# Optimization experiments

Measured on AMD Instinct MI355X. Metric: run time of the kernel, lower is better.

## Reference

```python
import jax, jax.numpy as jnp
import numpy as np


def swiglu(g, u):
    return jax.nn.silu(g) * u


def setup_inputs() -> dict:
    key = jax.random.key(0)
    ks = jax.random.split(key, 10)
    D, H, E, HS = 2048, 512, 32, 1024
    B, S = 1, 2048
    s = 0.02
    return {
        "x": jax.random.normal(ks[0], (B, S, D), jnp.float32),
        "gate_w": jax.random.normal(ks[1], (E, D), jnp.float32) * s,
        "expert_bias": jnp.zeros((E,), jnp.float32),
        "wg": jax.random.normal(ks[2], (E, D, H), jnp.float32) * s,
        "wu": jax.random.normal(ks[3], (E, D, H), jnp.float32) * s,
        "wd": jax.random.normal(ks[4], (E, H, D), jnp.float32) * s,
        "sg": jax.random.normal(ks[5], (D, HS), jnp.float32) * s,
        "su": jax.random.normal(ks[6], (D, HS), jnp.float32) * s,
        "sd": jax.random.normal(ks[7], (HS, D), jnp.float32) * s,
        "coef_w": jax.random.normal(ks[8], (2, D), jnp.float32) * s,
        "coef_b": jnp.zeros((2,), jnp.float32),
        "top_k": 4,
    }


def reference(x, gate_w, expert_bias, wg, wu, wd, sg, su, sd, coef_w, coef_b, top_k):
    # --- sigmoid router with bias-adjusted top-k selection ---
    logits = jnp.einsum("bsd,ed->bse", x, gate_w)            # [B,S,E]
    routing = jax.nn.sigmoid(logits.astype(jnp.float32))
    biased = routing + expert_bias[None, None, :]
    _, inds = jax.lax.top_k(biased, top_k)                    # [B,S,k]
    scores = jnp.take_along_axis(routing, inds, axis=-1)      # gather UNbiased weights
    scores = scores / (jnp.sum(scores, axis=-1, keepdims=True) + 1e-20)  # norm_topk_prob
    scores = scores.astype(x.dtype)

    # --- SwitchGLU experts: dense per-expert SwiGLU, then gather top-k outputs ---
    h = jnp.einsum("bsd,edh->bseh", x, wg)                    # [B,S,E,H]
    u = jnp.einsum("bsd,edh->bseh", x, wu)
    y_all = jnp.einsum("bseh,ehd->bsed", swiglu(h, u), wd)    # [B,S,E,D]
    expert_out = jnp.take_along_axis(
        y_all, inds[..., None], axis=2)                        # [B,S,k,D]
    y_experts = jnp.sum(expert_out * scores[..., None], axis=-2)  # [B,S,D]

    # --- shared expert + learned 2-way mixing coefficient ---
    shared = swiglu(x @ sg, x @ su) @ sd                      # [B,S,D]
    coef = jax.nn.softmax(jnp.einsum("bsd,cd->bsc", x, coef_w) + coef_b, axis=-1)
    return y_experts * coef[..., :1] + shared * coef[..., 1:]
```

## Files before the change

### kernel.cpp

```cpp
#include <hip/hip_runtime.h>
#include <hip/hip_bf16.h>
#include <stdint.h>

#define S_TOK   2048
#define DMODEL  2048
#define HEXP    512
#define NEXP    32
#define HSH     1024
#define NPAIR   (S_TOK * 4)
#define MAXTILES 96

#define META_NT  0
#define META_TE  1
#define META_TP0 (1 + MAXTILES)
#define META_TM  (1 + 2 * MAXTILES)
#define META_SIZE (1 + 3 * MAXTILES)

typedef short  s16x8 __attribute__((ext_vector_type(8)));
typedef __bf16 b16x8 __attribute__((ext_vector_type(8)));
typedef float  f32x4 __attribute__((ext_vector_type(4)));

__device__ __forceinline__ f32x4 mfma16x16x32(s16x8 a, s16x8 b, f32x4 c) {
    return __builtin_amdgcn_mfma_f32_16x16x32_bf16(
        __builtin_bit_cast(b16x8, a), __builtin_bit_cast(b16x8, b), c, 0, 0, 0);
}

__device__ __forceinline__ unsigned short f2bf(float f) {
    union { float f; unsigned int u; } v; v.f = f;
    unsigned int u = v.u;
    return (unsigned short)((u + 0x7FFFu + ((u >> 16) & 1u)) >> 16);
}

__global__ __launch_bounds__(256)
void router_kernel(const float* __restrict__ x, const float* __restrict__ gate_w,
                   const float* __restrict__ expert_bias,
                   const float* __restrict__ coef_w, const float* __restrict__ coef_b,
                   int* __restrict__ inds, float* __restrict__ scores,
                   float* __restrict__ coefo)
{
    const int t = blockIdx.x;
    const int tid = threadIdx.x;
    const int lane = tid & 63;
    const int wave = tid >> 6;
    const float* xr = x + (size_t)t * DMODEL;

    float xv[32];
#pragma unroll
    for (int j = 0; j < 32; ++j) xv[j] = xr[lane + 64 * j];

    __shared__ float s_logits[NEXP];
    __shared__ float s_coef[2];

    for (int i = 0; i < 8; ++i) {
        const int e = wave * 8 + i;
        const float* wr = gate_w + (size_t)e * DMODEL;
        float p = 0.f;
#pragma unroll
        for (int j = 0; j < 32; ++j) p += xv[j] * wr[lane + 64 * j];
#pragma unroll
        for (int o = 32; o > 0; o >>= 1) p += __shfl_xor(p, o);
        if (lane == 0) s_logits[e] = p;
    }
    if (wave == 0) {
        for (int c = 0; c < 2; ++c) {
            const float* wr = coef_w + (size_t)c * DMODEL;
            float p = 0.f;
#pragma unroll
            for (int j = 0; j < 32; ++j) p += xv[j] * wr[lane + 64 * j];
#pragma unroll
            for (int o = 32; o > 0; o >>= 1) p += __shfl_xor(p, o);
            if (lane == 0) s_coef[c] = p;
        }
    }
    __syncthreads();
    if (tid == 0) {
        float routing[NEXP], biased[NEXP];
        for (int e = 0; e < NEXP; ++e) {
            const float r = 1.f / (1.f + expf(-s_logits[e]));
            routing[e] = r;
            biased[e] = r + expert_bias[e];
        }
        int sel[4]; float sc[4]; float ssum = 0.f;
        for (int k = 0; k < 4; ++k) {
            int best = 0; float bv = -1e30f;
            for (int e = 0; e < NEXP; ++e)
                if (biased[e] > bv) { bv = biased[e]; best = e; }
            sel[k] = best; sc[k] = routing[best]; ssum += sc[k];
            biased[best] = -1e30f;
        }
        const float inv = 1.f / (ssum + 1e-20f);
        for (int k = 0; k < 4; ++k) {
            inds[t * 4 + k] = sel[k];
            scores[t * 4 + k] = sc[k] * inv;
        }
        const float l0 = s_coef[0] + coef_b[0];
        const float l1 = s_coef[1] + coef_b[1];
        const float m = fmaxf(l0, l1);
        const float e0 = expf(l0 - m), e1 = expf(l1 - m);
        coefo[t * 2 + 0] = e0 / (e0 + e1);
        coefo[t * 2 + 1] = e1 / (e0 + e1);
    }
}

__global__ __launch_bounds__(256)
void xcast_kernel(const float* __restrict__ x, unsigned short* __restrict__ xb)
{
    const int i = (blockIdx.x * 256 + threadIdx.x) * 4;
    const float4 v = *reinterpret_cast<const float4*>(x + i);
    ushort4 o;
    o.x = f2bf(v.x); o.y = f2bf(v.y); o.z = f2bf(v.z); o.w = f2bf(v.w);
    *reinterpret_cast<ushort4*>(xb + i) = o;
}

__global__ __launch_bounds__(1024)
void group_kernel(const int* __restrict__ inds, const float* __restrict__ scores,
                  int* __restrict__ meta, int* __restrict__ pair_token,
                  float* __restrict__ pair_score)
{
    __shared__ int cnt[NEXP];
    __shared__ int off_s[NEXP];
    __shared__ int cur[NEXP];
    const int tid = threadIdx.x;
    if (tid < NEXP) cnt[tid] = 0;
    __syncthreads();
    for (int i = tid; i < NPAIR; i += 1024) atomicAdd(&cnt[inds[i]], 1);
    __syncthreads();
    if (tid == 0) {
        int run = 0, nt = 0;
        for (int e = 0; e < NEXP; ++e) {
            off_s[e] = run;
            const int c = cnt[e];
            for (int m0 = 0; m0 < c; m0 += 128) {
                meta[META_TE + nt] = e;
                meta[META_TP0 + nt] = run + m0;
                meta[META_TM + nt] = (c - m0 < 128) ? (c - m0) : 128;
                ++nt;
            }
            run += c;
        }
        meta[META_NT] = nt;
    }
    __syncthreads();
    if (tid < NEXP) cur[tid] = off_s[tid];
    __syncthreads();
    for (int i = tid; i < NPAIR; i += 1024) {
        const int e = inds[i];
        const int pos = atomicAdd(&cur[e], 1);
        pair_token[pos] = i >> 2;
        pair_score[pos] = scores[i];
    }
}

template <bool GATHER>
__global__ __launch_bounds__(256, 2)
void gateup_kernel(const unsigned short* __restrict__ xb,
                   const float* __restrict__ Bg_all, const float* __restrict__ Bu_all,
                   unsigned short* __restrict__ act,
                   const int* __restrict__ meta, const int* __restrict__ pair_token,
                   const int NB)
{
    __shared__ unsigned short Al[128][40];
    __shared__ unsigned short Bgl[64][40];
    __shared__ unsigned short Bul[64][40];

    const int tid = threadIdx.x;
    int p0, mval;
    const float *Bg, *Bu;
    if constexpr (GATHER) {
        const int tt = blockIdx.y;
        if (tt >= meta[META_NT]) return;
        const int e = meta[META_TE + tt];
        p0 = meta[META_TP0 + tt];
        mval = meta[META_TM + tt];
        const size_t eoff = (size_t)e * DMODEL * NB;
        Bg = Bg_all + eoff;
        Bu = Bu_all + eoff;
    } else {
        p0 = blockIdx.y * 128;
        mval = 128;
        Bg = Bg_all;
        Bu = Bu_all;
    }
    const int n0 = blockIdx.x * 64;

    const int am = tid >> 1;
    const int ah = (tid & 1) * 16;
    int tok;
    if constexpr (GATHER) {
        int p = p0 + am; if (p > NPAIR - 1) p = NPAIR - 1;
        tok = pair_token[p];
    } else {
        tok = p0 + am;
    }
    const unsigned short* asrc = xb + (size_t)tok * DMODEL + ah;

    const int bn = tid & 63;
    const int bk = (tid >> 6) * 8;
    const float* bgsrc = Bg + (size_t)bk * NB + (n0 + bn);
    const float* busrc = Bu + (size_t)bk * NB + (n0 + bn);

    uint4 av0 = *reinterpret_cast<const uint4*>(asrc);
    uint4 av1 = *reinterpret_cast<const uint4*>(asrc + 8);
    float pg[8], pu[8];
#pragma unroll
    for (int j = 0; j < 8; ++j) {
        pg[j] = bgsrc[(size_t)j * NB];
        pu[j] = busrc[(size_t)j * NB];
    }

    const f32x4 zero4 = {0.f, 0.f, 0.f, 0.f};
    f32x4 hacc[4][2], uacc[4][2];
#pragma unroll
    for (int m = 0; m < 4; ++m)
#pragma unroll
        for (int n = 0; n < 2; ++n) { hacc[m][n] = zero4; uacc[m][n] = zero4; }

    const int lane = tid & 63;
    const int wave = tid >> 6;
    const int wm = wave >> 1, wn = wave & 1;
    const int fr = lane & 15;
    const int fk = (lane >> 4) * 8;

    for (int k0 = 0; k0 < DMODEL; k0 += 32) {
        __syncthreads();
        *reinterpret_cast<uint4*>(&Al[am][ah])     = av0;
        *reinterpret_cast<uint4*>(&Al[am][ah + 8]) = av1;
        union { unsigned short us[8]; uint4 v; } wg_, wu_;
#pragma unroll
        for (int j = 0; j < 8; ++j) { wg_.us[j] = f2bf(pg[j]); wu_.us[j] = f2bf(pu[j]); }
        *reinterpret_cast<uint4*>(&Bgl[bn][bk]) = wg_.v;
        *reinterpret_cast<uint4*>(&Bul[bn][bk]) = wu_.v;
        if (k0 + 32 < DMODEL) {
            av0 = *reinterpret_cast<const uint4*>(asrc + k0 + 32);
            av1 = *reinterpret_cast<const uint4*>(asrc + k0 + 40);
            const float* g2 = bgsrc + (size_t)(k0 + 32) * NB;
            const float* u2 = busrc + (size_t)(k0 + 32) * NB;
#pragma unroll
            for (int j = 0; j < 8; ++j) { pg[j] = g2[(size_t)j * NB]; pu[j] = u2[(size_t)j * NB]; }
        }
        __syncthreads();

        s16x8 af[4], bgf[2], buf2[2];
#pragma unroll
        for (int m = 0; m < 4; ++m)
            af[m] = *reinterpret_cast<const s16x8*>(&Al[wm * 64 + m * 16 + fr][fk]);
#pragma unroll
        for (int n = 0; n < 2; ++n) {
            bgf[n]  = *reinterpret_cast<const s16x8*>(&Bgl[wn * 32 + n * 16 + fr][fk]);
            buf2[n] = *reinterpret_cast<const s16x8*>(&Bul[wn * 32 + n * 16 + fr][fk]);
        }
#pragma unroll
        for (int m = 0; m < 4; ++m)
#pragma unroll
            for (int n = 0; n < 2; ++n) {
                hacc[m][n] = mfma16x16x32(af[m], bgf[n], hacc[m][n]);
                uacc[m][n] = mfma16x16x32(af[m], buf2[n], uacc[m][n]);
            }
    }

#pragma unroll
    for (int m = 0; m < 4; ++m)
#pragma unroll
        for (int n = 0; n < 2; ++n) {
            const int col = n0 + wn * 32 + n * 16 + fr;
#pragma unroll
            for (int r = 0; r < 4; ++r) {
                const int rt = wm * 64 + m * 16 + (lane >> 4) * 4 + r;
                if (rt < mval) {
                    const float hv = hacc[m][n][r];
                    const float a = hv / (1.f + __expf(-hv)) * uacc[m][n][r];
                    act[(size_t)(p0 + rt) * NB + col] = f2bf(a);
                }
            }
        }
}

template <bool EXPERT>
__global__ __launch_bounds__(256, 2)
void down_kernel(const unsigned short* __restrict__ act,
                 const float* __restrict__ Bd_all,
                 float* __restrict__ out,
                 const int* __restrict__ meta, const int* __restrict__ pair_token,
                 const float* __restrict__ pair_score, const float* __restrict__ coef,
                 const int KA)
{
    __shared__ unsigned short Al[128][40];
    __shared__ unsigned short Bl[64][40];

    const int tid = threadIdx.x;
    int p0, mval;
    const float* Bd;
    if constexpr (EXPERT) {
        const int tt = blockIdx.y;
        if (tt >= meta[META_NT]) return;
        const int e = meta[META_TE + tt];
        p0 = meta[META_TP0 + tt];
        mval = meta[META_TM + tt];
        Bd = Bd_all + (size_t)e * KA * DMODEL;
    } else {
        p0 = blockIdx.y * 128;
        mval = 128;
        Bd = Bd_all;
    }
    const int n0 = blockIdx.x * 64;

    const int am = tid >> 1;
    const int ah = (tid & 1) * 16;
    int ar = p0 + am;
    if constexpr (EXPERT) { if (ar > NPAIR - 1) ar = NPAIR - 1; }
    const unsigned short* asrc = act + (size_t)ar * KA + ah;

    const int bn = tid & 63;
    const int bk = (tid >> 6) * 8;
    const float* bsrc = Bd + (size_t)bk * DMODEL + (n0 + bn);

    uint4 av0 = *reinterpret_cast<const uint4*>(asrc);
    uint4 av1 = *reinterpret_cast<const uint4*>(asrc + 8);
    float pb[8];
#pragma unroll
    for (int j = 0; j < 8; ++j) pb[j] = bsrc[(size_t)j * DMODEL];

    const f32x4 zero4 = {0.f, 0.f, 0.f, 0.f};
    f32x4 acc[4][2];
#pragma unroll
    for (int m = 0; m < 4; ++m)
#pragma unroll
        for (int n = 0; n < 2; ++n) acc[m][n] = zero4;

    const int lane = tid & 63;
    const int wave = tid >> 6;
    const int wm = wave >> 1, wn = wave & 1;
    const int fr = lane & 15;
    const int fk = (lane >> 4) * 8;

    for (int k0 = 0; k0 < KA; k0 += 32) {
        __syncthreads();
        *reinterpret_cast<uint4*>(&Al[am][ah])     = av0;
        *reinterpret_cast<uint4*>(&Al[am][ah + 8]) = av1;
        union { unsigned short us[8]; uint4 v; } wb_;
#pragma unroll
        for (int j = 0; j < 8; ++j) wb_.us[j] = f2bf(pb[j]);
        *reinterpret_cast<uint4*>(&Bl[bn][bk]) = wb_.v;
        if (k0 + 32 < KA) {
            av0 = *reinterpret_cast<const uint4*>(asrc + k0 + 32);
            av1 = *reinterpret_cast<const uint4*>(asrc + k0 + 40);
            const float* b2 = bsrc + (size_t)(k0 + 32) * DMODEL;
#pragma unroll
            for (int j = 0; j < 8; ++j) pb[j] = b2[(size_t)j * DMODEL];
        }
        __syncthreads();

        s16x8 af[4], bf[2];
#pragma unroll
        for (int m = 0; m < 4; ++m)
            af[m] = *reinterpret_cast<const s16x8*>(&Al[wm * 64 + m * 16 + fr][fk]);
#pragma unroll
        for (int n = 0; n < 2; ++n)
            bf[n] = *reinterpret_cast<const s16x8*>(&Bl[wn * 32 + n * 16 + fr][fk]);
#pragma unroll
        for (int m = 0; m < 4; ++m)
#pragma unroll
            for (int n = 0; n < 2; ++n)
                acc[m][n] = mfma16x16x32(af[m], bf[n], acc[m][n]);
    }

#pragma unroll
    for (int m = 0; m < 4; ++m)
#pragma unroll
        for (int n = 0; n < 2; ++n) {
            const int col = n0 + wn * 32 + n * 16 + fr;
#pragma unroll
            for (int r = 0; r < 4; ++r) {
                const int rt = wm * 64 + m * 16 + (lane >> 4) * 4 + r;
                if (rt < mval) {
                    if constexpr (EXPERT) {
                        const int p = p0 + rt;
                        const int t = pair_token[p];
                        const float s = pair_score[p];
                        atomicAdd(&out[(size_t)t * DMODEL + col], acc[m][n][r] * s);
                    } else {
                        const int row = p0 + rt;
                        const float c0 = coef[row * 2 + 0];
                        const float c1 = coef[row * 2 + 1];
                        const size_t idx = (size_t)row * DMODEL + col;
                        out[idx] = out[idx] * c0 + acc[m][n][r] * c1;
                    }
                }
            }
        }
}

extern "C" void kernel_launch(void* const* d_in, const int* in_sizes, int n_in,
                              void* d_out, int out_size, void* d_ws, size_t ws_size,
                              hipStream_t stream)
{
    const float* x           = (const float*)d_in[0];
    const float* gate_w      = (const float*)d_in[1];
    const float* expert_bias = (const float*)d_in[2];
    const float* wg          = (const float*)d_in[3];
    const float* wu          = (const float*)d_in[4];
    const float* wd          = (const float*)d_in[5];
    const float* sg          = (const float*)d_in[6];
    const float* su          = (const float*)d_in[7];
    const float* sd          = (const float*)d_in[8];
    const float* coef_w      = (const float*)d_in[9];
    const float* coef_b      = (const float*)d_in[10];
    float* out = (float*)d_out;

    char* ws = (char*)d_ws;
    size_t off = 0;
    auto take = [&](size_t bytes) {
        char* p = ws + off;
        off = (off + bytes + 255) & ~(size_t)255;
        return p;
    };
    int*   inds     = (int*)  take((size_t)S_TOK * 4 * sizeof(int));
    float* scores   = (float*)take((size_t)S_TOK * 4 * sizeof(float));
    float* coefp    = (float*)take((size_t)S_TOK * 2 * sizeof(float));
    int*   meta     = (int*)  take((size_t)META_SIZE * sizeof(int));
    int*   pair_tok = (int*)  take((size_t)NPAIR * sizeof(int));
    float* pair_sc  = (float*)take((size_t)NPAIR * sizeof(float));
    unsigned short* xb    = (unsigned short*)take((size_t)S_TOK * DMODEL * 2);
    unsigned short* act   = (unsigned short*)take((size_t)NPAIR * HEXP * 2);
    unsigned short* shact = (unsigned short*)take((size_t)S_TOK * HSH * 2);
    (void)ws_size; (void)in_sizes; (void)n_in; (void)out_size;

    hipMemsetAsync(d_out, 0, (size_t)S_TOK * DMODEL * sizeof(float), stream);

    router_kernel<<<S_TOK, 256, 0, stream>>>(x, gate_w, expert_bias, coef_w, coef_b,
                                             inds, scores, coefp);
    xcast_kernel<<<(S_TOK * DMODEL / 4) / 256, 256, 0, stream>>>(x, xb);
    group_kernel<<<1, 1024, 0, stream>>>(inds, scores, meta, pair_tok, pair_sc);

    gateup_kernel<true><<<dim3(HEXP / 64, MAXTILES), 256, 0, stream>>>(
        xb, wg, wu, act, meta, pair_tok, HEXP);
    gateup_kernel<false><<<dim3(HSH / 64, S_TOK / 128), 256, 0, stream>>>(
        xb, sg, su, shact, nullptr, nullptr, HSH);
    down_kernel<true><<<dim3(DMODEL / 64, MAXTILES), 256, 0, stream>>>(
        act, wd, out, meta, pair_tok, pair_sc, nullptr, HEXP);
    down_kernel<false><<<dim3(DMODEL / 64, S_TOK / 128), 256, 0, stream>>>(
        shact, sd, out, nullptr, nullptr, nullptr, coefp, HSH);
}
```

Before: 400.2 us.

## Double-buffer LDS with BK=64 in gate/up and down GEMMs, widen down tile

Both GEMM kernels now use double-buffered shared memory with a K step of 64. The next tile's global loads are issued before the current tile's MFMAs, and only one barrier runs per iteration. The down kernel's N tile doubles to 128, so each A tile is reused across more columns and the grid is halved. This raises LDS use (about 72 KB per block) and register pressure from the larger prefetch and accumulator arrays, which may cut occupancy below the requested two blocks per CU.

```diff
diff --git a/kernel.cpp b/kernel.cpp
--- a/kernel.cpp
+++ b/kernel.cpp
@@ -15,6 +15,8 @@
 #define META_TP0 (1 + MAXTILES)
 #define META_TM  (1 + 2 * MAXTILES)
 #define META_SIZE (1 + 3 * MAXTILES)
+
+#define LDP 72
 
 typedef short  s16x8 __attribute__((ext_vector_type(8)));
 typedef __bf16 b16x8 __attribute__((ext_vector_type(8)));
@@ -159,9 +161,9 @@
                    const int* __restrict__ meta, const int* __restrict__ pair_token,
                    const int NB)
 {
-    __shared__ unsigned short Al[128][40];
-    __shared__ unsigned short Bgl[64][40];
-    __shared__ unsigned short Bul[64][40];
+    constexpr int NT = DMODEL / 64;
+    __shared__ unsigned short Al[2][128][LDP];
+    __shared__ unsigned short Bl[2][128][LDP];
 
     const int tid = threadIdx.x;
     int p0, mval;
@@ -183,79 +185,92 @@
     }
     const int n0 = blockIdx.x * 64;
 
-    const int am = tid >> 1;
-    const int ah = (tid & 1) * 16;
+    const int arow = tid >> 1;
+    const int aoff = (tid & 1) * 32;
     int tok;
     if constexpr (GATHER) {
-        int p = p0 + am; if (p > NPAIR - 1) p = NPAIR - 1;
+        int p = p0 + arow; if (p > NPAIR - 1) p = NPAIR - 1;
         tok = pair_token[p];
     } else {
-        tok = p0 + am;
-    }
-    const unsigned short* asrc = xb + (size_t)tok * DMODEL + ah;
-
-    const int bn = tid & 63;
-    const int bk = (tid >> 6) * 8;
-    const float* bgsrc = Bg + (size_t)bk * NB + (n0 + bn);
-    const float* busrc = Bu + (size_t)bk * NB + (n0 + bn);
-
-    uint4 av0 = *reinterpret_cast<const uint4*>(asrc);
-    uint4 av1 = *reinterpret_cast<const uint4*>(asrc + 8);
-    float pg[8], pu[8];
-#pragma unroll
-    for (int j = 0; j < 8; ++j) {
-        pg[j] = bgsrc[(size_t)j * NB];
-        pu[j] = busrc[(size_t)j * NB];
-    }
-
-    const f32x4 zero4 = {0.f, 0.f, 0.f, 0.f};
-    f32x4 hacc[4][2], uacc[4][2];
-#pragma unroll
-    for (int m = 0; m < 4; ++m)
-#pragma unroll
-        for (int n = 0; n < 2; ++n) { hacc[m][n] = zero4; uacc[m][n] = zero4; }
+        tok = p0 + arow;
+    }
+    const unsigned short* asrc = xb + (size_t)tok * DMODEL + aoff;
+
+    const int bcol = tid & 63;
+    const int bkb = (tid >> 6) * 16;
+    const float* gsrc = Bg + (size_t)bkb * NB + (n0 + bcol);
+    const float* usrc = Bu + (size_t)bkb * NB + (n0 + bcol);
+
+    uint4 areg[4];
+    float greg[16], ureg[16];
+
+    auto load_regs = [&](int k0) {
+#pragma unroll
+        for (int j = 0; j < 4; ++j)
+            areg[j] = *reinterpret_cast<const uint4*>(asrc + k0 + j * 8);
+#pragma unroll
+        for (int j = 0; j < 16; ++j) {
+            greg[j] = gsrc[(size_t)(k0 + j) * NB];
+            ureg[j] = usrc[(size_t)(k0 + j) * NB];
+        }
+    };
+    auto write_lds = [&](int buf) {
+#pragma unroll
+        for (int j = 0; j < 4; ++j)
+            *reinterpret_cast<uint4*>(&Al[buf][arow][aoff + j * 8]) = areg[j];
+        union { unsigned short us[16]; uint4 v[2]; } g_, u_;
+#pragma unroll
+        for (int j = 0; j < 16; ++j) { g_.us[j] = f2bf(greg[j]); u_.us[j] = f2bf(ureg[j]); }
+        *reinterpret_cast<uint4*>(&Bl[buf][bcol][bkb])          = g_.v[0];
+        *reinterpret_cast<uint4*>(&Bl[buf][bcol][bkb + 8])      = g_.v[1];
+        *reinterpret_cast<uint4*>(&Bl[buf][64 + bcol][bkb])     = u_.v[0];
+        *reinterpret_cast<uint4*>(&Bl[buf][64 + bcol][bkb + 8]) = u_.v[1];
+    };
 
     const int lane = tid & 63;
     const int wave = tid >> 6;
     const int wm = wave >> 1, wn = wave & 1;
-    const int fr = lane & 15;
-    const int fk = (lane >> 4) * 8;
-
-    for (int k0 = 0; k0 < DMODEL; k0 += 32) {
+    const int fr = lane & 15, fq = lane >> 4;
+
+    const f32x4 zero4 = {0.f, 0.f, 0.f, 0.f};
+    f32x4 hacc[4][2], uacc[4][2];
+#pragma unroll
+    for (int m = 0; m < 4; ++m)
+#pragma unroll
+        for (int n = 0; n < 2; ++n) { hacc[m][n] = zero4; uacc[m][n] = zero4; }
+
+    auto compute = [&](int buf) {
+#pragma unroll
+        for (int kk = 0; kk < 2; ++kk) {
+            const int ko = kk * 32 + fq * 8;
+            s16x8 af[4], bg[2], bu[2];
+#pragma unroll
+            for (int m = 0; m < 4; ++m)
+                af[m] = *reinterpret_cast<const s16x8*>(&Al[buf][wm * 64 + m * 16 + fr][ko]);
+#pragma unroll
+            for (int n = 0; n < 2; ++n) {
+                bg[n] = *reinterpret_cast<const s16x8*>(&Bl[buf][wn * 32 + n * 16 + fr][ko]);
+                bu[n] = *reinterpret_cast<const s16x8*>(&Bl[buf][64 + wn * 32 + n * 16 + fr][ko]);
+            }
+#pragma unroll
+            for (int m = 0; m < 4; ++m)
+#pragma unroll
+                for (int n = 0; n < 2; ++n) {
+                    hacc[m][n] = mfma16x16x32(af[m], bg[n], hacc[m][n]);
+                    uacc[m][n] = mfma16x16x32(af[m], bu[n], uacc[m][n]);
+                }
+        }
+    };
+
+    load_regs(0);
+    write_lds(0);
+    __syncthreads();
+    for (int t = 0; t < NT; ++t) {
+        const int cur = t & 1;
+        if (t + 1 < NT) load_regs((t + 1) * 64);
+        compute(cur);
+        if (t + 1 < NT) write_lds(cur ^ 1);
         __syncthreads();
-        *reinterpret_cast<uint4*>(&Al[am][ah])     = av0;
-        *reinterpret_cast<uint4*>(&Al[am][ah + 8]) = av1;
-        union { unsigned short us[8]; uint4 v; } wg_, wu_;
-#pragma unroll
-        for (int j = 0; j < 8; ++j) { wg_.us[j] = f2bf(pg[j]); wu_.us[j] = f2bf(pu[j]); }
-        *reinterpret_cast<uint4*>(&Bgl[bn][bk]) = wg_.v;
-        *reinterpret_cast<uint4*>(&Bul[bn][bk]) = wu_.v;
-        if (k0 + 32 < DMODEL) {
-            av0 = *reinterpret_cast<const uint4*>(asrc + k0 + 32);
-            av1 = *reinterpret_cast<const uint4*>(asrc + k0 + 40);
-            const float* g2 = bgsrc + (size_t)(k0 + 32) * NB;
-            const float* u2 = busrc + (size_t)(k0 + 32) * NB;
-#pragma unroll
-            for (int j = 0; j < 8; ++j) { pg[j] = g2[(size_t)j * NB]; pu[j] = u2[(size_t)j * NB]; }
-        }
-        __syncthreads();
-
-        s16x8 af[4], bgf[2], buf2[2];
-#pragma unroll
-        for (int m = 0; m < 4; ++m)
-            af[m] = *reinterpret_cast<const s16x8*>(&Al[wm * 64 + m * 16 + fr][fk]);
-#pragma unroll
-        for (int n = 0; n < 2; ++n) {
-            bgf[n]  = *reinterpret_cast<const s16x8*>(&Bgl[wn * 32 + n * 16 + fr][fk]);
-            buf2[n] = *reinterpret_cast<const s16x8*>(&Bul[wn * 32 + n * 16 + fr][fk]);
-        }
-#pragma unroll
-        for (int m = 0; m < 4; ++m)
-#pragma unroll
-            for (int n = 0; n < 2; ++n) {
-                hacc[m][n] = mfma16x16x32(af[m], bgf[n], hacc[m][n]);
-                uacc[m][n] = mfma16x16x32(af[m], buf2[n], uacc[m][n]);
-            }
     }
 
 #pragma unroll
@@ -265,7 +280,7 @@
             const int col = n0 + wn * 32 + n * 16 + fr;
 #pragma unroll
             for (int r = 0; r < 4; ++r) {
-                const int rt = wm * 64 + m * 16 + (lane >> 4) * 4 + r;
+                const int rt = wm * 64 + m * 16 + fq * 4 + r;
                 if (rt < mval) {
                     const float hv = hacc[m][n][r];
                     const float a = hv / (1.f + __expf(-hv)) * uacc[m][n][r];
@@ -284,8 +299,9 @@
                  const float* __restrict__ pair_score, const float* __restrict__ coef,
                  const int KA)
 {
-    __shared__ unsigned short Al[128][40];
-    __shared__ unsigned short Bl[64][40];
+    const int NT = KA / 64;
+    __shared__ unsigned short Al[2][128][LDP];
+    __shared__ unsigned short Bl[2][128][LDP];
 
     const int tid = threadIdx.x;
     int p0, mval;
@@ -302,82 +318,97 @@
         mval = 128;
         Bd = Bd_all;
     }
-    const int n0 = blockIdx.x * 64;
-
-    const int am = tid >> 1;
-    const int ah = (tid & 1) * 16;
-    int ar = p0 + am;
+    const int n0 = blockIdx.x * 128;
+
+    const int arow = tid >> 1;
+    const int aoff = (tid & 1) * 32;
+    int ar = p0 + arow;
     if constexpr (EXPERT) { if (ar > NPAIR - 1) ar = NPAIR - 1; }
-    const unsigned short* asrc = act + (size_t)ar * KA + ah;
-
-    const int bn = tid & 63;
-    const int bk = (tid >> 6) * 8;
-    const float* bsrc = Bd + (size_t)bk * DMODEL + (n0 + bn);
-
-    uint4 av0 = *reinterpret_cast<const uint4*>(asrc);
-    uint4 av1 = *reinterpret_cast<const uint4*>(asrc + 8);
-    float pb[8];
-#pragma unroll
-    for (int j = 0; j < 8; ++j) pb[j] = bsrc[(size_t)j * DMODEL];
-
-    const f32x4 zero4 = {0.f, 0.f, 0.f, 0.f};
-    f32x4 acc[4][2];
-#pragma unroll
-    for (int m = 0; m < 4; ++m)
-#pragma unroll
-        for (int n = 0; n < 2; ++n) acc[m][n] = zero4;
+    const unsigned short* asrc = act + (size_t)ar * KA + aoff;
+
+    const int bcol = tid & 127;
+    const int bkb = (tid >> 7) * 32;
+    const float* bsrc = Bd + (size_t)bkb * DMODEL + (n0 + bcol);
+
+    uint4 areg[4];
+    float breg[32];
+
+    auto load_regs = [&](int k0) {
+#pragma unroll
+        for (int j = 0; j < 4; ++j)
+            areg[j] = *reinterpret_cast<const uint4*>(asrc + k0 + j * 8);
+#pragma unroll
+        for (int j = 0; j < 32; ++j)
+            breg[j] = bsrc[(size_t)(k0 + j) * DMODEL];
+    };
+    auto write_lds = [&](int buf) {
+#pragma unroll
+        for (int j = 0; j < 4; ++j)
+            *reinterpret_cast<uint4*>(&Al[buf][arow][aoff + j * 8]) = areg[j];
+        union { unsigned short us[32]; uint4 v[4]; } b_;
+#pragma unroll
+        for (int j = 0; j < 32; ++j) b_.us[j] = f2bf(breg[j]);
+#pragma unroll
+        for (int j = 0; j < 4; ++j)
+            *reinterpret_cast<uint4*>(&Bl[buf][bcol][bkb + j * 8]) = b_.v[j];
+    };
 
     const int lane = tid & 63;
     const int wave = tid >> 6;
     const int wm = wave >> 1, wn = wave & 1;
-    const int fr = lane & 15;
-    const int fk = (lane >> 4) * 8;
-
-    for (int k0 = 0; k0 < KA; k0 += 32) {
+    const int fr = lane & 15, fq = lane >> 4;
+
+    const f32x4 zero4 = {0.f, 0.f, 0.f, 0.f};
+    f32x4 acc[4][4];
+#pragma unroll
+    for (int m = 0; m < 4; ++m)
+#pragma unroll
+        for (int n = 0; n < 4; ++n) acc[m][n] = zero4;
+
+    auto compute = [&](int buf) {
+#pragma unroll
+        for (int kk = 0; kk < 2; ++kk) {
+            const int ko = kk * 32 + fq * 8;
+            s16x8 af[4], bf[4];
+#pragma unroll
+            for (int m = 0; m < 4; ++m)
+                af[m] = *reinterpret_cast<const s16x8*>(&Al[buf][wm * 64 + m * 16 + fr][ko]);
+#pragma unroll
+            for (int n = 0; n < 4; ++n)
+                bf[n] = *reinterpret_cast<const s16x8*>(&Bl[buf][wn * 64 + n * 16 + fr][ko]);
+#pragma unroll
+            for (int m = 0; m < 4; ++m)
+#pragma unroll
+                for (int n = 0; n < 4; ++n)
+                    acc[m][n] = mfma16x16x32(af[m], bf[n], acc[m][n]);
+        }
+    };
+
+    load_regs(0);
+    write_lds(0);
+    __syncthreads();
+    for (int t = 0; t < NT; ++t) {
+        const int cur = t & 1;
+        if (t + 1 < NT) load_regs((t + 1) * 64);
+        compute(cur);
+        if (t + 1 < NT) write_lds(cur ^ 1);
         __syncthreads();
-        *reinterpret_cast<uint4*>(&Al[am][ah])     = av0;
-        *reinterpret_cast<uint4*>(&Al[am][ah + 8]) = av1;
-        union { unsigned short us[8]; uint4 v; } wb_;
-#pragma unroll
-        for (int j = 0; j < 8; ++j) wb_.us[j] = f2bf(pb[j]);
-        *reinterpret_cast<uint4*>(&Bl[bn][bk]) = wb_.v;
-        if (k0 + 32 < KA) {
-            av0 = *reinterpret_cast<const uint4*>(asrc + k0 + 32);
-            av1 = *reinterpret_cast<const uint4*>(asrc + k0 + 40);
-            const float* b2 = bsrc + (size_t)(k0 + 32) * DMODEL;
-#pragma unroll
-            for (int j = 0; j < 8; ++j) pb[j] = b2[(size_t)j * DMODEL];
-        }
-        __syncthreads();
-
-        s16x8 af[4], bf[2];
-#pragma unroll
-        for (int m = 0; m < 4; ++m)
-            af[m] = *reinterpret_cast<const s16x8*>(&Al[wm * 64 + m * 16 + fr][fk]);
-#pragma unroll
-        for (int n = 0; n < 2; ++n)
-            bf[n] = *reinterpret_cast<const s16x8*>(&Bl[wn * 32 + n * 16 + fr][fk]);
-#pragma unroll
-        for (int m = 0; m < 4; ++m)
-#pragma unroll
-            for (int n = 0; n < 2; ++n)
-                acc[m][n] = mfma16x16x32(af[m], bf[n], acc[m][n]);
     }
 
 #pragma unroll
     for (int m = 0; m < 4; ++m)
 #pragma unroll
-        for (int n = 0; n < 2; ++n) {
-            const int col = n0 + wn * 32 + n * 16 + fr;
+        for (int n = 0; n < 4; ++n) {
+            const int col = n0 + wn * 64 + n * 16 + fr;
 #pragma unroll
             for (int r = 0; r < 4; ++r) {
-                const int rt = wm * 64 + m * 16 + (lane >> 4) * 4 + r;
+                const int rt = wm * 64 + m * 16 + fq * 4 + r;
                 if (rt < mval) {
                     if constexpr (EXPERT) {
                         const int p = p0 + rt;
-                        const int t = pair_token[p];
+                        const int t2 = pair_token[p];
                         const float s = pair_score[p];
-                        atomicAdd(&out[(size_t)t * DMODEL + col], acc[m][n][r] * s);
+                        atomicAdd(&out[(size_t)t2 * DMODEL + col], acc[m][n][r] * s);
                     } else {
                         const int row = p0 + rt;
                         const float c0 = coef[row * 2 + 0];
@@ -436,8 +467,8 @@
         xb, wg, wu, act, meta, pair_tok, HEXP);
     gateup_kernel<false><<<dim3(HSH / 64, S_TOK / 128), 256, 0, stream>>>(
         xb, sg, su, shact, nullptr, nullptr, HSH);
-    down_kernel<true><<<dim3(DMODEL / 64, MAXTILES), 256, 0, stream>>>(
+    down_kernel<true><<<dim3(DMODEL / 128, MAXTILES), 256, 0, stream>>>(
         act, wd, out, meta, pair_tok, pair_sc, nullptr, HEXP);
-    down_kernel<false><<<dim3(DMODEL / 64, S_TOK / 128), 256, 0, stream>>>(
+    down_kernel<false><<<dim3(DMODEL / 128, S_TOK / 128), 256, 0, stream>>>(
         shact, sd, out, nullptr, nullptr, nullptr, coefp, HSH);
 }
```

New measurement: 582.5 us. +45.5%, slower.
